# Kernel tuning notes

Hardware: AMD Instinct MI355X
Metric: run time of the kernel (lower is better)

## Reference

```python
import jax, jax.numpy as jnp
import numpy as np

B, N, F, G, H = 8, 1024, 512, 128, 8
D = F // H  # head_dim = 64


def setup_inputs() -> dict:
    key = jax.random.key(0)
    ks = jax.random.split(key, 24)
    def lin(k, fan_in, shape):
        return jax.random.normal(k, shape, jnp.float32) / np.sqrt(fan_in)
    return {
        "features": jax.random.normal(ks[0], (B, N, F), jnp.float32),
        "geometry": jax.random.normal(ks[1], (B, N, G), jnp.float32),
        "coords": jax.random.normal(ks[2], (B, N, 3), jnp.float32),
        # nnx.MultiHeadAttention params (q/k/v/out dense, with bias)
        "wq": lin(ks[3], F, (F, F)), "bq": jnp.zeros((F,), jnp.float32),
        "wk": lin(ks[4], F, (F, F)), "bk": jnp.zeros((F,), jnp.float32),
        "wv": lin(ks[5], F, (F, F)), "bv": jnp.zeros((F,), jnp.float32),
        "wo": lin(ks[6], F, (F, F)), "bo": jnp.zeros((F,), jnp.float32),
        # geometry q/k/v linears
        "gq_w": lin(ks[7], G, (G, F)), "gq_b": jnp.zeros((F,), jnp.float32),
        "gk_w": lin(ks[8], G, (G, F)), "gk_b": jnp.zeros((F,), jnp.float32),
        "gv_w": lin(ks[9], G, (G, F)), "gv_b": jnp.zeros((F,), jnp.float32),
        # distance MLP: Linear(1->H), gelu, Linear(H->H)
        "d1_w": lin(ks[10], 1, (1, H)), "d1_b": jnp.zeros((H,), jnp.float32),
        "d2_w": lin(ks[11], H, (H, H)), "d2_b": jnp.zeros((H,), jnp.float32),
        # output projection
        "op_w": lin(ks[12], F, (F, F)), "op_b": jnp.zeros((F,), jnp.float32),
    }


def _forward(features, geometry, coords,
             wq, bq, wk, bk, wv, bv, wo, bo,
             gq_w, gq_b, gk_w, gk_b, gv_w, gv_b,
             d1_w, d1_b, d2_w, d2_b, op_w, op_b):
    scale = jnp.sqrt(jnp.float32(D))
    # --- standard multi-head self-attention branch (nnx.MultiHeadAttention) ---
    q = (features @ wq + bq).reshape(B, N, H, D)
    k = (features @ wk + bk).reshape(B, N, H, D)
    v = (features @ wv + bv).reshape(B, N, H, D)
    scores = jnp.einsum("bqhd,bkhd->bhqk", q, k) / scale
    attn = jax.nn.softmax(scores, axis=-1)
    feat_att = jnp.einsum("bhqk,bkhd->bqhd", attn, v).reshape(B, N, F)
    feat_att = feat_att @ wo + bo
    # --- geometry attention branch ---
    gq = geometry @ gq_w + gq_b
    gk = geometry @ gk_w + gk_b
    gv = geometry @ gv_w + gv_b
    g_scores = jnp.einsum("bqd,bkd->bqk", gq, gk) / scale
    # pairwise distances (B,N,N,1); clamp for sqrt-at-zero safety (diagonal)
    diff = coords[:, :, None, :] - coords[:, None, :, :]
    dist = jnp.sqrt(jnp.maximum(jnp.sum(diff * diff, -1, keepdims=True), 1e-12))
    dw = jax.nn.gelu(dist @ d1_w + d1_b) @ d2_w + d2_b  # (B,N,N,H)
    # transpose to (B,H,N,N) then mean over heads == mean over last axis
    g_scores = g_scores + jnp.mean(dw, axis=-1)
    g_attn = jax.nn.softmax(g_scores, axis=-1)
    geom_att = jnp.einsum("bqk,bkd->bqd", g_attn, gv)
    return (feat_att + geom_att) @ op_w + op_b


def reference(features, geometry, coords,
              wq, bq, wk, bk, wv, bv, wo, bo,
              gq_w, gq_b, gk_w, gk_b, gv_w, gv_b,
              d1_w, d1_b, d2_w, d2_b, op_w, op_b):
    return _forward(features, geometry, coords,
                    wq, bq, wk, bk, wv, bv, wo, bo,
                    gq_w, gq_b, gk_w, gk_b, gv_w, gv_b,
                    d1_w, d1_b, d2_w, d2_b, op_w, op_b)
```

## Files before the change

### kernel.cpp

```cpp
#include <hip/hip_runtime.h>

typedef __bf16 bf16_t;
typedef __bf16 bf16x8 __attribute__((ext_vector_type(8)));
typedef __bf16 bf16x4v __attribute__((ext_vector_type(4)));
typedef float f32x4 __attribute__((ext_vector_type(4)));

#define MFMA16(a, b, c) __builtin_amdgcn_mfma_f32_16x16x32_bf16((a), (b), (c), 0, 0, 0)

static constexpr int B_ = 8, N_ = 1024, F_ = 512, H_ = 8;
static constexpr int M_ = B_ * N_;
static constexpr float LOG2E = 1.4426950408889634f;

__device__ __forceinline__ void gl_lds16(const bf16_t* gsrc, bf16_t* ldst) {
  __builtin_amdgcn_global_load_lds(
      (const __attribute__((address_space(1))) void*)gsrc,
      (__attribute__((address_space(3))) void*)ldst, 16, 0, 0);
}

__device__ __forceinline__ float gelu_tanh(float u) {
  float g = 0.7978845608028654f * fmaf(0.044715f * u * u, u, u);
  float e = __expf(2.f * g);
  float t = 1.f - 2.f / (e + 1.f);
  return 0.5f * u * (1.f + t);
}

struct PrepArgs {
  const float *features, *geometry;
  const float *wq, *wk, *wv, *wo, *op_w;
  const float *gq_w, *gk_w, *gv_w;
  const float *bq, *bk, *bv, *gq_b, *gv_b;
  const float *d1w, *d1b, *d2w, *d2b;
  bf16_t *featBF, *geomBF, *gkwBF, *WqkvT, *GqvT, *WoT, *OpT;
  float *bqkv, *gqvb, *dlut;
};

static constexpr int PR_C0 = 4096;
static constexpr int PR_C1 = PR_C0 + 1024;
static constexpr int PR_GKC = PR_C1 + 64;
static constexpr int PR_WQ = PR_GKC + 256;
static constexpr int PR_WK = PR_WQ + 256;
static constexpr int PR_WV = PR_WK + 256;
static constexpr int PR_WO = PR_WV + 256;
static constexpr int PR_OP = PR_WO + 256;
static constexpr int PR_GQ = PR_OP + 64;
static constexpr int PR_GV = PR_GQ + 64;
static constexpr int PR_B1 = PR_GV + 6;
static constexpr int PR_B2 = PR_B1 + 4;
static constexpr int PR_LUT = PR_B2 + 16;
static constexpr int PR_TOTAL = PR_LUT;

__device__ __forceinline__ void prep_cast(const float* __restrict__ in,
                                          bf16_t* __restrict__ out, int blk) {
  int i = blk * 256 + threadIdx.x;
  float4 v = ((const float4*)in)[i];
  bf16x4v o;
  o[0] = (bf16_t)v.x; o[1] = (bf16_t)v.y; o[2] = (bf16_t)v.z; o[3] = (bf16_t)v.w;
  ((bf16x4v*)out)[i] = o;
}

__device__ __forceinline__ void prep_transpose(const float* __restrict__ W,
                                               bf16_t* __restrict__ Wt,
                                               int K, int N, int ldo, int idx,
                                               float (*t)[33]) {
  const int bx = idx & 15, by = idx >> 4;
  const int kb = by * 32, cb = bx * 32;
  const int tx = threadIdx.x & 31, ty = threadIdx.x >> 5;
#pragma unroll
  for (int i = 0; i < 4; ++i)
    t[ty * 4 + i][tx] = W[(long)(kb + ty * 4 + i) * N + cb + tx];
  __syncthreads();
#pragma unroll
  for (int i = 0; i < 4; ++i)
    Wt[(long)(cb + ty * 4 + i) * ldo + kb + tx] = (bf16_t)t[tx][ty * 4 + i];
}

__global__ __launch_bounds__(256) void k_prep(PrepArgs p) {
  __shared__ float tsh[32][33];
  const int blk = blockIdx.x;
  if (blk < PR_C0) {
    prep_cast(p.features, p.featBF, blk);
  } else if (blk < PR_C1) {
    prep_cast(p.geometry, p.geomBF, blk - PR_C0);
  } else if (blk < PR_GKC) {
    prep_cast(p.gk_w, p.gkwBF, blk - PR_C1);
  } else if (blk < PR_WQ) {
    prep_transpose(p.wq, p.WqkvT, 512, 512, 512, blk - PR_GKC, tsh);
  } else if (blk < PR_WK) {
    prep_transpose(p.wk, p.WqkvT + 512 * 512, 512, 512, 512, blk - PR_WQ, tsh);
  } else if (blk < PR_WV) {
    prep_transpose(p.wv, p.WqkvT + 1024 * 512, 512, 512, 512, blk - PR_WK, tsh);
  } else if (blk < PR_WO) {
    prep_transpose(p.wo, p.WoT, 512, 512, 512, blk - PR_WV, tsh);
  } else if (blk < PR_OP) {
    prep_transpose(p.op_w, p.OpT, 512, 512, 512, blk - PR_WO, tsh);
  } else if (blk < PR_GQ) {
    prep_transpose(p.gq_w, p.GqvT, 128, 512, 128, blk - PR_OP, tsh);
  } else if (blk < PR_GV) {
    prep_transpose(p.gv_w, p.GqvT + 512 * 128, 128, 512, 128, blk - PR_GQ, tsh);
  } else if (blk < PR_B1) {
    int i = (blk - PR_GV) * 256 + threadIdx.x;
    p.bqkv[i] = i < 512 ? p.bq[i] : (i < 1024 ? p.bk[i - 512] : p.bv[i - 1024]);
  } else if (blk < PR_B2) {
    int i = (blk - PR_B1) * 256 + threadIdx.x;
    p.gqvb[i] = i < 512 ? p.gq_b[i] : p.gv_b[i - 512];
  } else {
    int i = (blk - PR_B2) * 256 + threadIdx.x;
    float d = (i + 0.5f) * (16.f / 4096.f);
    float s = 0.f;
#pragma unroll
    for (int h = 0; h < 8; ++h) s += p.d2b[h];
    s *= 0.125f;
#pragma unroll
    for (int j = 0; j < 8; ++j) {
      float w2 = 0.f;
#pragma unroll
      for (int h = 0; h < 8; ++h) w2 += p.d2w[j * 8 + h];
      s = fmaf(gelu_tanh(fmaf(d, p.d1w[j], p.d1b[j])), w2 * 0.125f, s);
    }
    p.dlut[i] = s;
  }
}

struct GemmArgs {
  const bf16_t* A; const bf16_t* Bt;
  const float* bias; const float* addSrc; const bf16_t* addSrcB;
  const float* coords; const float* lut;
  float* outF; bf16_t* outB;
  bf16_t* outT;
  int vtileFrom;
  long strideAb; long strideBb;
  int lda, ldb, K, ldout;
  float scale;
};

__device__ __forceinline__ void gemm128_core(const GemmArgs& g, int mBase, int cBase,
                                             bf16_t (*As)[64], bf16_t (*Bs)[64]) {
  const int tid = threadIdx.x;
  const int w = tid >> 6, lane = tid & 63;
  const int lr = lane & 15, lg = lane >> 4;
  const int wr = w >> 1, wc = w & 1;
  const int batch = mBase >> 10;

  const int srow = lane >> 3;
  const int scol = (lane & 7) * 8;
  const bf16_t* Ag = g.A + (long)batch * g.strideAb +
                     (long)((mBase & 1023) + w * 32 + srow) * g.lda + scol;
  const bf16_t* Bg = g.Bt + (long)batch * g.strideBb +
                     (long)(cBase + w * 32 + srow) * g.ldb + scol;
  bf16_t* Al = &As[w * 32][0];
  bf16_t* Bl = &Bs[w * 32][0];

  f32x4 zero = {0.f, 0.f, 0.f, 0.f};
  f32x4 acc[4][4];
#pragma unroll
  for (int i = 0; i < 4; ++i)
#pragma unroll
    for (int j = 0; j < 4; ++j) acc[i][j] = zero;

  for (int k0 = 0; k0 < g.K; k0 += 64) {
#pragma unroll
    for (int is = 0; is < 4; ++is) {
      gl_lds16(Ag + (long)(is * 8) * g.lda + k0, Al + is * 8 * 64);
      gl_lds16(Bg + (long)(is * 8) * g.ldb + k0, Bl + is * 8 * 64);
    }
    __syncthreads();
#pragma unroll
    for (int ks = 0; ks < 2; ++ks) {
      bf16x8 a[4], b[4];
#pragma unroll
      for (int i = 0; i < 4; ++i) {
        a[i] = *(const bf16x8*)(&As[wr * 64 + i * 16 + lr][ks * 32 + lg * 8]);
        b[i] = *(const bf16x8*)(&Bs[wc * 64 + i * 16 + lr][ks * 32 + lg * 8]);
      }
#pragma unroll
      for (int mf = 0; mf < 4; ++mf)
#pragma unroll
        for (int nf = 0; nf < 4; ++nf)
          acc[mf][nf] = MFMA16(a[mf], b[nf], acc[mf][nf]);
    }
    __syncthreads();
  }

  const int c0 = cBase + wc * 64;
  float bias4[4];
#pragma unroll
  for (int nf = 0; nf < 4; ++nf)
    bias4[nf] = g.bias ? g.bias[c0 + nf * 16 + lr] : 0.f;
  const bool vtile = (g.outT != nullptr) && (cBase >= g.vtileFrom);
#pragma unroll
  for (int mf = 0; mf < 4; ++mf) {
    const int r0 = mBase + wr * 64 + mf * 16 + lg * 4;
    const int r0b = r0 & 1023;
#pragma unroll
    for (int nf = 0; nf < 4; ++nf) {
      const int c = c0 + nf * 16 + lr;
      if (vtile) {
        bf16x4v vv;
#pragma unroll
        for (int rg = 0; rg < 4; ++rg)
          vv[rg] = (bf16_t)(acc[mf][nf][rg] * g.scale + bias4[nf]);
        *(bf16x4v*)(&g.outT[((long)batch * 512 + (c - g.vtileFrom)) * 1024 + r0b]) = vv;
      } else {
#pragma unroll
        for (int rg = 0; rg < 4; ++rg) {
          const int r = r0 + rg;
          float v = acc[mf][nf][rg] * g.scale + bias4[nf];
          if (g.addSrc) v += g.addSrc[(long)r * g.ldout + c];
          const long oi = (long)r * g.ldout + c;
          if (g.outF) g.outF[oi] = v;
          if (g.outB) g.outB[oi] = (bf16_t)v;
        }
      }
    }
  }
}

__global__ __launch_bounds__(256) void k_gemm128_dual(GemmArgs g1, GemmArgs g2) {
  __shared__ alignas(16) bf16_t As[128][64];
  __shared__ alignas(16) bf16_t Bs[128][64];
  const int bx = blockIdx.x;
  if (bx < 768) {
    gemm128_core(g1, (bx / 12) * 128, (bx % 12) * 128, As, Bs);
  } else {
    const int i = bx - 768;
    gemm128_core(g2, (i / 8) * 128, (i % 8) * 128, As, Bs);
  }
}

__device__ __forceinline__ void gemm128_dist(const GemmArgs& g, int mBase, int cBase,
                                             char* smemc) {
  bf16_t (*As)[64] = (bf16_t (*)[64])smemc;
  bf16_t (*Bs)[64] = (bf16_t (*)[64])(smemc + 16384);
  bf16_t* Lut = (bf16_t*)(smemc + 32768);
  const int tid = threadIdx.x;
  const int w = tid >> 6, lane = tid & 63;
  const int lr = lane & 15, lg = lane >> 4;
  const int wr = w >> 1, wc = w & 1;
  const int batch = mBase >> 10;

  {
    const float4* src = (const float4*)g.lut;
#pragma unroll
    for (int i = 0; i < 4; ++i) {
      float4 v = src[tid + i * 256];
      bf16x4v o;
      o[0] = (bf16_t)(v.x * LOG2E); o[1] = (bf16_t)(v.y * LOG2E);
      o[2] = (bf16_t)(v.z * LOG2E); o[3] = (bf16_t)(v.w * LOG2E);
      ((bf16x4v*)Lut)[tid + i * 256] = o;
    }
  }

  const int srow = lane >> 3;
  const int scol = (lane & 7) * 8;
  const bf16_t* Ag = g.A + (long)batch * g.strideAb +
                     (long)((mBase & 1023) + w * 32 + srow) * g.lda + scol;
  const bf16_t* Bg = g.Bt + (long)batch * g.strideBb +
                     (long)(cBase + w * 32 + srow) * g.ldb + scol;
  bf16_t* Al = &As[w * 32][0];
  bf16_t* Bl = &Bs[w * 32][0];

  f32x4 zero = {0.f, 0.f, 0.f, 0.f};
  f32x4 acc[4][4];
#pragma unroll
  for (int i = 0; i < 4; ++i)
#pragma unroll
    for (int j = 0; j < 4; ++j) acc[i][j] = zero;

  for (int k0 = 0; k0 < g.K; k0 += 64) {
#pragma unroll
    for (int is = 0; is < 4; ++is) {
      gl_lds16(Ag + (long)(is * 8) * g.lda + k0, Al + is * 8 * 64);
      gl_lds16(Bg + (long)(is * 8) * g.ldb + k0, Bl + is * 8 * 64);
    }
    __syncthreads();
#pragma unroll
    for (int ks = 0; ks < 2; ++ks) {
      bf16x8 a[4], b[4];
#pragma unroll
      for (int i = 0; i < 4; ++i) {
        a[i] = *(const bf16x8*)(&As[wr * 64 + i * 16 + lr][ks * 32 + lg * 8]);
        b[i] = *(const bf16x8*)(&Bs[wc * 64 + i * 16 + lr][ks * 32 + lg * 8]);
      }
#pragma unroll
      for (int mf = 0; mf < 4; ++mf)
#pragma unroll
        for (int nf = 0; nf < 4; ++nf)
          acc[mf][nf] = MFMA16(a[mf], b[nf], acc[mf][nf]);
    }
    __syncthreads();
  }

  const int c0 = cBase + wc * 64;
  float ckx[4], cky[4], ckz[4];
#pragma unroll
  for (int nf = 0; nf < 4; ++nf) {
    const float* ck = g.coords + ((long)batch * 1024 + c0 + nf * 16 + lr) * 3;
    ckx[nf] = ck[0]; cky[nf] = ck[1]; ckz[nf] = ck[2];
  }
#pragma unroll
  for (int mf = 0; mf < 4; ++mf) {
    const int r0 = mBase + wr * 64 + mf * 16 + lg * 4;
    float cqx[4], cqy[4], cqz[4];
#pragma unroll
    for (int rg = 0; rg < 4; ++rg) {
      const float* cq = g.coords + ((long)batch * 1024 + ((r0 + rg) & 1023)) * 3;
      cqx[rg] = cq[0]; cqy[rg] = cq[1]; cqz[rg] = cq[2];
    }
#pragma unroll
    for (int nf = 0; nf < 4; ++nf) {
      const int c = c0 + nf * 16 + lr;
#pragma unroll
      for (int rg = 0; rg < 4; ++rg) {
        const int r = r0 + rg;
        float v = acc[mf][nf][rg] * g.scale;
        float dx = cqx[rg] - ckx[nf], dy = cqy[rg] - cky[nf], dz = cqz[rg] - ckz[nf];
        float d = sqrtf(fmaxf(dx * dx + dy * dy + dz * dz, 1e-12f));
        int idx = (int)(d * 256.f);
        idx = idx > 4095 ? 4095 : idx;
        g.outB[(long)r * g.ldout + c] = (bf16_t)exp2f(v + (float)Lut[idx]);
      }
    }
  }
}

__device__ __forceinline__ void flash_core(const bf16_t* __restrict__ QKV,
                                           const bf16_t* __restrict__ Vt,
                                           bf16_t* __restrict__ fatt,
                                           int qx, int bh, char* smemc) {
  bf16_t (*Ks)[64][64] = (bf16_t (*)[64][64])smemc;
  bf16_t (*Vs)[64][64] = (bf16_t (*)[64][64])(smemc + 16384);
  char* Plb = smemc + 32768;
  const int wave = threadIdx.x >> 6, lane = threadIdx.x & 63;
  const int lr = lane & 15, lg = (lane >> 4) & 3;
  const int b = bh >> 3, h = bh & 7;
  const int qbase = qx * 64 + wave * 16;

  const bf16_t* Qb = QKV + (long)b * 1024 * 1536 + h * 64;
  const bf16_t* Kb = Qb + 512;
  const bf16_t* Vg = Vt + ((long)b * 512 + h * 64) * 1024;

  constexpr float SCL = 0.18033688011112042f;
  bf16x8 q_[2];
#pragma unroll
  for (int dh = 0; dh < 2; ++dh) {
    bf16x8 raw = *(const bf16x8*)(Qb + (long)(qbase + lr) * 1536 + dh * 32 + lg * 8);
#pragma unroll
    for (int j = 0; j < 8; ++j) q_[dh][j] = (bf16_t)((float)raw[j] * SCL);
  }
  bf16x8 onesb;
#pragma unroll
  for (int j = 0; j < 8; ++j) onesb[j] = (bf16_t)1.0f;

  const int srow = lane >> 3;
  const int scol = (((lane & 7) ^ srow) << 3);
  const bf16_t* KgB = Kb + (long)(wave * 16 + srow) * 1536 + scol;
  const bf16_t* VgB = Vg + (long)(wave * 16 + srow) * 1024 + scol;

  auto stage = [&](int buf, int kt) {
#pragma unroll
    for (int i = 0; i < 2; ++i) {
      gl_lds16(KgB + (long)(kt + i * 8) * 1536, &Ks[buf][wave * 16 + i * 8][0]);
      gl_lds16(VgB + (long)(i * 8) * 1024 + kt, &Vs[buf][wave * 16 + i * 8][0]);
    }
  };

  f32x4 zero = {0.f, 0.f, 0.f, 0.f};
  f32x4 oacc[4] = {zero, zero, zero, zero};
  f32x4 oL = zero;
  const int swz = (lr & 7) << 4;
  char* PlW = Plb + wave * 1280;

  stage(0, 0);
  asm volatile("s_waitcnt vmcnt(0)" ::: "memory");
  __syncthreads();

  auto tile = [&](const int buf, int t) __attribute__((always_inline)) {
    if (t < 15) stage(buf ^ 1, (t + 1) * 64);
    const char* KB = (const char*)&Ks[buf][0][0];
    const char* VB = (const char*)&Vs[buf][0][0];
#pragma unroll
    for (int kk = 0; kk < 2; ++kk) {
      f32x4 S[2];
      __builtin_amdgcn_s_setprio(1);
#pragma unroll
      for (int kh = 0; kh < 2; ++kh) {
        const int row = kk * 32 + kh * 16 + lr;
        bf16x8 k0 = *(const bf16x8*)(KB + row * 128 + ((lg * 16) ^ swz));
        bf16x8 k1 = *(const bf16x8*)(KB + row * 128 + ((64 + lg * 16) ^ swz));
        f32x4 tt = MFMA16(k0, q_[0], zero);
        S[kh] = MFMA16(k1, q_[1], tt);
      }
      __builtin_amdgcn_s_setprio(0);
#pragma unroll
      for (int kh = 0; kh < 2; ++kh) {
        bf16x4v pp;
#pragma unroll
        for (int r = 0; r < 4; ++r) pp[r] = (bf16_t)exp2f(S[kh][r]);
        *(bf16x4v*)(PlW + lr * 80 + kh * 32 + lg * 8) = pp;
      }
      asm volatile("s_waitcnt lgkmcnt(0)" ::: "memory");
      const bf16x8 pa = *(const bf16x8*)(PlW + lr * 80 + lg * 16);
      __builtin_amdgcn_s_setprio(1);
#pragma unroll
      for (int ct = 0; ct < 4; ++ct) {
        const int vrow = ct * 16 + lr;
        bf16x8 vf = *(const bf16x8*)(VB + vrow * 128 + ((kk * 64 + lg * 16) ^ swz));
        oacc[ct] = MFMA16(pa, vf, oacc[ct]);
      }
      oL = MFMA16(pa, onesb, oL);
      __builtin_amdgcn_s_setprio(0);
    }
    asm volatile("s_waitcnt vmcnt(0)" ::: "memory");
    __syncthreads();
  };

  for (int tt = 0; tt < 8; ++tt) {
    tile(0, tt * 2);
    tile(1, tt * 2 + 1);
  }

#pragma unroll
  for (int r = 0; r < 4; ++r) {
    float inv = 1.f / oL[r];
    int q = qbase + lg * 4 + r;
    bf16_t* orow = fatt + ((long)b * 1024 + q) * 512 + h * 64;
#pragma unroll
    for (int ct = 0; ct < 4; ++ct)
      orow[ct * 16 + lr] = (bf16_t)(oacc[ct][r] * inv);
  }
}

__global__ __launch_bounds__(256) void k_gsc_flash(GemmArgs g,
                                                   const bf16_t* __restrict__ QKV,
                                                   const bf16_t* __restrict__ Vt,
                                                   bf16_t* __restrict__ fatt) {
  __shared__ alignas(16) char smem[40960];
  const int bx = blockIdx.x;
  if (bx < 512) {
    gemm128_dist(g, (bx >> 3) * 128, (bx & 7) * 128, smem);
  } else {
    const int fid = bx - 512;
    flash_core(QKV, Vt, fatt, fid & 15, fid >> 4, smem);
  }
}

template <int RSUM>
__device__ __forceinline__ void m64_loop(const GemmArgs& g, int mBase, int cBase,
                                         bf16_t (*As)[64], bf16_t (*Bs)[64],
                                         f32x4 (*acc)[2], f32x4* lacc) {
  const int tid = threadIdx.x;
  const int w = tid >> 6, lane = tid & 63;
  const int lr = lane & 15, lg = lane >> 4;
  const int wr = w >> 1, wc = w & 1;
  const int batch = mBase >> 10;

  const int srow = lane >> 3;
  const int scol = (lane & 7) * 8;
  const bf16_t* Ag = g.A + (long)batch * g.strideAb +
                     (long)((mBase & 1023) + w * 16 + srow) * g.lda + scol;
  const bf16_t* Bg = g.Bt + (long)batch * g.strideBb +
                     (long)(cBase + w * 16 + srow) * g.ldb + scol;
  bf16_t* Al = &As[w * 16][0];
  bf16_t* Bl = &Bs[w * 16][0];

  bf16x8 onesb;
#pragma unroll
  for (int j = 0; j < 8; ++j) onesb[j] = (bf16_t)1.0f;

  for (int k0 = 0; k0 < g.K; k0 += 64) {
#pragma unroll
    for (int is = 0; is < 2; ++is) {
      gl_lds16(Ag + (long)(is * 8) * g.lda + k0, Al + is * 8 * 64);
      gl_lds16(Bg + (long)(is * 8) * g.ldb + k0, Bl + is * 8 * 64);
    }
    __syncthreads();
#pragma unroll
    for (int ks = 0; ks < 2; ++ks) {
      bf16x8 a[2], b[2];
#pragma unroll
      for (int i = 0; i < 2; ++i) {
        a[i] = *(const bf16x8*)(&As[wr * 32 + i * 16 + lr][ks * 32 + lg * 8]);
        b[i] = *(const bf16x8*)(&Bs[wc * 32 + i * 16 + lr][ks * 32 + lg * 8]);
      }
#pragma unroll
      for (int mf = 0; mf < 2; ++mf)
#pragma unroll
        for (int nf = 0; nf < 2; ++nf)
          acc[mf][nf] = MFMA16(a[mf], b[nf], acc[mf][nf]);
      if constexpr (RSUM) {
#pragma unroll
        for (int mf = 0; mf < 2; ++mf)
          lacc[mf] = MFMA16(a[mf], onesb, lacc[mf]);
      }
    }
    __syncthreads();
  }
}

__global__ __launch_bounds__(256) void k_gemm_m64(GemmArgs g) {
  __shared__ alignas(16) bf16_t As[64][64];
  __shared__ alignas(16) bf16_t Bs[64][64];
  const int tid = threadIdx.x;
  const int w = tid >> 6, lane = tid & 63;
  const int lr = lane & 15, lg = lane >> 4;
  const int wr = w >> 1, wc = w & 1;
  const int mBase = blockIdx.y * 64, cBase = blockIdx.x * 64;

  f32x4 zero = {0.f, 0.f, 0.f, 0.f};
  f32x4 acc[2][2] = {{zero, zero}, {zero, zero}};
  m64_loop<0>(g, mBase, cBase, As, Bs, acc, nullptr);

  const int c0 = cBase + wc * 32;
  float bias2[2];
#pragma unroll
  for (int nf = 0; nf < 2; ++nf)
    bias2[nf] = g.bias ? g.bias[c0 + nf * 16 + lr] : 0.f;
#pragma unroll
  for (int mf = 0; mf < 2; ++mf) {
    const int r0 = mBase + wr * 32 + mf * 16 + lg * 4;
#pragma unroll
    for (int nf = 0; nf < 2; ++nf) {
      const int c = c0 + nf * 16 + lr;
#pragma unroll
      for (int rg = 0; rg < 4; ++rg) {
        const int r = r0 + rg;
        float v = acc[mf][nf][rg] * g.scale + bias2[nf];
        const long oi = (long)r * g.ldout + c;
        if (g.outF) g.outF[oi] = v;
        if (g.outB) g.outB[oi] = (bf16_t)v;
      }
    }
  }
}

__global__ __launch_bounds__(256) void k_comb(GemmArgs gF, GemmArgs gG,
                                              bf16_t* __restrict__ outB) {
  __shared__ alignas(16) bf16_t As[64][64];
  __shared__ alignas(16) bf16_t Bs[64][64];
  const int tid = threadIdx.x;
  const int w = tid >> 6, lane = tid & 63;
  const int lr = lane & 15, lg = lane >> 4;
  const int wr = w >> 1, wc = w & 1;
  const int mBase = blockIdx.y * 64, cBase = blockIdx.x * 64;

  f32x4 zero = {0.f, 0.f, 0.f, 0.f};
  f32x4 acc1[2][2] = {{zero, zero}, {zero, zero}};
  f32x4 acc2[2][2] = {{zero, zero}, {zero, zero}};
  f32x4 lacc[2] = {zero, zero};
  m64_loop<0>(gF, mBase, cBase, As, Bs, acc1, nullptr);
  m64_loop<1>(gG, mBase, cBase, As, Bs, acc2, lacc);

  const int c0 = cBase + wc * 32;
  float bias2[2];
#pragma unroll
  for (int nf = 0; nf < 2; ++nf)
    bias2[nf] = gF.bias[c0 + nf * 16 + lr];
#pragma unroll
  for (int mf = 0; mf < 2; ++mf) {
    const int r0 = mBase + wr * 32 + mf * 16 + lg * 4;
    float linv[4];
#pragma unroll
    for (int rg = 0; rg < 4; ++rg) linv[rg] = 1.f / lacc[mf][rg];
#pragma unroll
    for (int nf = 0; nf < 2; ++nf) {
      const int c = c0 + nf * 16 + lr;
#pragma unroll
      for (int rg = 0; rg < 4; ++rg) {
        const int r = r0 + rg;
        float v = acc2[mf][nf][rg] * linv[rg] + acc1[mf][nf][rg] + bias2[nf];
        outB[(long)r * 512 + c] = (bf16_t)v;
      }
    }
  }
}

extern "C" void kernel_launch(void* const* d_in, const int* in_sizes, int n_in,
                              void* d_out, int out_size, void* d_ws, size_t ws_size,
                              hipStream_t stream) {
  const float* features = (const float*)d_in[0];
  const float* geometry = (const float*)d_in[1];
  const float* coords   = (const float*)d_in[2];
  const float* wq = (const float*)d_in[3];  const float* bq = (const float*)d_in[4];
  const float* wk = (const float*)d_in[5];  const float* bk = (const float*)d_in[6];
  const float* wv = (const float*)d_in[7];  const float* bv = (const float*)d_in[8];
  const float* wo = (const float*)d_in[9];  const float* bo = (const float*)d_in[10];
  const float* gq_w = (const float*)d_in[11]; const float* gq_b = (const float*)d_in[12];
  const float* gk_w = (const float*)d_in[13]; const float* gk_b = (const float*)d_in[14];
  const float* gv_w = (const float*)d_in[15]; const float* gv_b = (const float*)d_in[16];
  const float* d1_w = (const float*)d_in[17]; const float* d1_b = (const float*)d_in[18];
  const float* d2_w = (const float*)d_in[19]; const float* d2_b = (const float*)d_in[20];
  const float* op_w = (const float*)d_in[21]; const float* op_b = (const float*)d_in[22];
  (void)gk_b;

  size_t off = 0;
  auto carve = [&](size_t bytes) {
    void* p = (char*)d_ws + off;
    off += (bytes + 255) & ~(size_t)255;
    return p;
  };
  bf16_t* featBF = (bf16_t*)carve((size_t)M_ * F_ * 2);
  bf16_t* geomBF = (bf16_t*)carve((size_t)M_ * 128 * 2);
  bf16_t* gkwBF  = (bf16_t*)carve((size_t)128 * 512 * 2);
  bf16_t* WqkvT  = (bf16_t*)carve((size_t)1536 * 512 * 2);
  bf16_t* GqvT   = (bf16_t*)carve((size_t)1024 * 128 * 2);
  bf16_t* WoT    = (bf16_t*)carve((size_t)512 * 512 * 2);
  bf16_t* OpT    = (bf16_t*)carve((size_t)512 * 512 * 2);
  float*  bqkv   = (float*)carve(1536 * 4);
  float*  gqvb   = (float*)carve(1024 * 4);
  float*  dlut   = (float*)carve(4096 * 4);
  bf16_t* QKV    = (bf16_t*)carve((size_t)M_ * 1536 * 2);
  bf16_t* GQV    = (bf16_t*)carve((size_t)M_ * 1024 * 2);
  bf16_t* GQeff  = (bf16_t*)carve((size_t)M_ * 128 * 2);
  bf16_t* Vt     = (bf16_t*)carve((size_t)B_ * 512 * 1024 * 2);
  bf16_t* GVt    = (bf16_t*)carve((size_t)B_ * 512 * 1024 * 2);
  bf16_t* Pun    = (bf16_t*)carve((size_t)M_ * 1024 * 2);
  bf16_t* fatt   = (bf16_t*)carve((size_t)M_ * 512 * 2);
  bf16_t* combB  = (bf16_t*)carve((size_t)M_ * 512 * 2);
  if (off > ws_size) return;

  PrepArgs p;
  p.features = features; p.geometry = geometry;
  p.wq = wq; p.wk = wk; p.wv = wv; p.wo = wo; p.op_w = op_w;
  p.gq_w = gq_w; p.gk_w = gk_w; p.gv_w = gv_w;
  p.bq = bq; p.bk = bk; p.bv = bv; p.gq_b = gq_b; p.gv_b = gv_b;
  p.d1w = d1_w; p.d1b = d1_b; p.d2w = d2_w; p.d2b = d2_b;
  p.featBF = featBF; p.geomBF = geomBF; p.gkwBF = gkwBF; p.WqkvT = WqkvT;
  p.GqvT = GqvT; p.WoT = WoT; p.OpT = OpT;
  p.bqkv = bqkv; p.gqvb = gqvb; p.dlut = dlut;
  k_prep<<<PR_TOTAL, 256, 0, stream>>>(p);

  auto mk = [](const bf16_t* A, long sAb, int lda, const bf16_t* Bt, long sBb, int ldb,
               int K, const float* bias, const float* addSrc, const bf16_t* addSrcB,
               float* outF, bf16_t* outB, int ldout, float scale,
               const float* coords, const float* lut, bf16_t* outT, int vtileFrom) {
    GemmArgs g;
    g.A = A; g.Bt = Bt; g.bias = bias; g.addSrc = addSrc; g.addSrcB = addSrcB;
    g.coords = coords; g.lut = lut; g.outF = outF; g.outB = outB; g.outT = outT;
    g.vtileFrom = vtileFrom;
    g.strideAb = sAb; g.strideBb = sBb; g.lda = lda; g.ldb = ldb;
    g.K = K; g.ldout = ldout; g.scale = scale;
    return g;
  };

  k_gemm128_dual<<<1280, 256, 0, stream>>>(
      mk(featBF, (long)1024 * 512, 512, WqkvT, 0, 512, 512,
         bqkv, nullptr, nullptr, nullptr, QKV, 1536, 1.f, nullptr, nullptr, Vt, 1024),
      mk(geomBF, (long)1024 * 128, 128, GqvT, 0, 128, 128,
         gqvb, nullptr, nullptr, nullptr, GQV, 1024, 1.f, nullptr, nullptr, GVt, 512));
  k_gemm_m64<<<dim3(2, 128), 256, 0, stream>>>(
      mk(GQV, (long)1024 * 1024, 1024, gkwBF, 0, 512, 512,
         nullptr, nullptr, nullptr, nullptr, GQeff, 128, 1.f, nullptr, nullptr,
         nullptr, 1 << 30));
  k_gsc_flash<<<1536, 256, 0, stream>>>(
      mk(GQeff, (long)1024 * 128, 128, geomBF, (long)1024 * 128, 128, 128,
         nullptr, nullptr, nullptr, nullptr, Pun, 1024, 0.125f * LOG2E,
         coords, dlut, nullptr, 1 << 30),
      QKV, Vt, fatt);
  k_comb<<<dim3(8, 128), 256, 0, stream>>>(
      mk(fatt, (long)1024 * 512, 512, WoT, 0, 512, 512,
         bo, nullptr, nullptr, nullptr, nullptr, 512, 1.f, nullptr, nullptr,
         nullptr, 1 << 30),
      mk(Pun, (long)1024 * 1024, 1024, GVt, (long)512 * 1024, 1024, 1024,
         nullptr, nullptr, nullptr, nullptr, nullptr, 512, 1.f, nullptr, nullptr,
         nullptr, 1 << 30),
      combB);
  k_gemm_m64<<<dim3(8, 128), 256, 0, stream>>>(
      mk(combB, (long)1024 * 512, 512, OpT, 0, 512, 512,
         op_b, nullptr, nullptr, (float*)d_out, nullptr, 512, 1.f, nullptr, nullptr,
         nullptr, 1 << 30));
}
```

Baseline: 166.7 us.

## Fold gq and gk weights into a single 128x128 effective projection

Precomputes Weff = gk_w·gq_wᵀ and beff = gk_w·gq_b inside the prep kernel with a small MFMA tile GEMM. The geometry query then projects directly to a 128-wide GQeff in the dual GEMM alongside GV, instead of materialising a 512-wide GQ and running a separate GEMM back down to 128. This removes one kernel launch, the GQV intermediate buffer and most of the geometry projection FLOPs. The cost is extra prep work, and rounding the folded weights to bf16 changes numerics slightly.

```diff
diff --git a/kernel.cpp b/kernel.cpp
--- a/kernel.cpp
+++ b/kernel.cpp
@@ -30,22 +30,22 @@
   const float *gq_w, *gk_w, *gv_w;
   const float *bq, *bk, *bv, *gq_b, *gv_b;
   const float *d1w, *d1b, *d2w, *d2b;
-  bf16_t *featBF, *geomBF, *gkwBF, *WqkvT, *GqvT, *WoT, *OpT;
-  float *bqkv, *gqvb, *dlut;
+  bf16_t *featBF, *geomBF, *WqkvT, *GqvT2, *WoT, *OpT;
+  float *bqkv, *gqvb2, *dlut;
 };
 
 static constexpr int PR_C0 = 4096;
 static constexpr int PR_C1 = PR_C0 + 1024;
-static constexpr int PR_GKC = PR_C1 + 64;
-static constexpr int PR_WQ = PR_GKC + 256;
+static constexpr int PR_WQ = PR_C1 + 256;
 static constexpr int PR_WK = PR_WQ + 256;
 static constexpr int PR_WV = PR_WK + 256;
 static constexpr int PR_WO = PR_WV + 256;
 static constexpr int PR_OP = PR_WO + 256;
-static constexpr int PR_GQ = PR_OP + 64;
-static constexpr int PR_GV = PR_GQ + 64;
-static constexpr int PR_B1 = PR_GV + 6;
-static constexpr int PR_B2 = PR_B1 + 4;
+static constexpr int PR_GVT = PR_OP + 64;
+static constexpr int PR_WEFF = PR_GVT + 4;
+static constexpr int PR_BEFF = PR_WEFF + 1;
+static constexpr int PR_B1 = PR_BEFF + 6;
+static constexpr int PR_B2 = PR_B1 + 2;
 static constexpr int PR_LUT = PR_B2 + 16;
 static constexpr int PR_TOTAL = PR_LUT;
 
@@ -74,17 +74,23 @@
     Wt[(long)(cb + ty * 4 + i) * ldo + kb + tx] = (bf16_t)t[tx][ty * 4 + i];
 }
 
+__device__ __forceinline__ bf16x8 cvt2x4(float4 a, float4 b) {
+  bf16x8 v;
+  v[0] = (bf16_t)a.x; v[1] = (bf16_t)a.y; v[2] = (bf16_t)a.z; v[3] = (bf16_t)a.w;
+  v[4] = (bf16_t)b.x; v[5] = (bf16_t)b.y; v[6] = (bf16_t)b.z; v[7] = (bf16_t)b.w;
+  return v;
+}
+
 __global__ __launch_bounds__(256) void k_prep(PrepArgs p) {
-  __shared__ float tsh[32][33];
+  __shared__ alignas(16) char psh[16384];
+  float (*tsh)[33] = (float (*)[33])psh;
   const int blk = blockIdx.x;
   if (blk < PR_C0) {
     prep_cast(p.features, p.featBF, blk);
   } else if (blk < PR_C1) {
     prep_cast(p.geometry, p.geomBF, blk - PR_C0);
-  } else if (blk < PR_GKC) {
-    prep_cast(p.gk_w, p.gkwBF, blk - PR_C1);
   } else if (blk < PR_WQ) {
-    prep_transpose(p.wq, p.WqkvT, 512, 512, 512, blk - PR_GKC, tsh);
+    prep_transpose(p.wq, p.WqkvT, 512, 512, 512, blk - PR_C1, tsh);
   } else if (blk < PR_WK) {
     prep_transpose(p.wk, p.WqkvT + 512 * 512, 512, 512, 512, blk - PR_WQ, tsh);
   } else if (blk < PR_WV) {
@@ -93,16 +99,73 @@
     prep_transpose(p.wo, p.WoT, 512, 512, 512, blk - PR_WV, tsh);
   } else if (blk < PR_OP) {
     prep_transpose(p.op_w, p.OpT, 512, 512, 512, blk - PR_WO, tsh);
-  } else if (blk < PR_GQ) {
-    prep_transpose(p.gq_w, p.GqvT, 128, 512, 128, blk - PR_OP, tsh);
-  } else if (blk < PR_GV) {
-    prep_transpose(p.gv_w, p.GqvT + 512 * 128, 128, 512, 128, blk - PR_GQ, tsh);
+  } else if (blk < PR_GVT) {
+    prep_transpose(p.gv_w, p.GqvT2 + 128 * 128, 128, 512, 128, blk - PR_OP, tsh);
+  } else if (blk < PR_WEFF) {
+    bf16_t (*As)[64] = (bf16_t (*)[64])psh;
+    bf16_t (*Bs)[64] = (bf16_t (*)[64])(psh + 8192);
+    const int wb = blk - PR_GVT;
+    const int gBrow = (wb >> 1) * 64;
+    const int hBcol = (wb & 1) * 64;
+    const int tid = threadIdx.x;
+    const int w4 = tid >> 6, lane = tid & 63;
+    const int lr = lane & 15, lg = lane >> 4;
+    const int wr = w4 >> 1, wc = w4 & 1;
+    const int srow = tid >> 2, scol = (tid & 3) << 4;
+    f32x4 zero = {0.f, 0.f, 0.f, 0.f};
+    f32x4 acc[2][2] = {{zero, zero}, {zero, zero}};
+    for (int f0 = 0; f0 < 512; f0 += 64) {
+#pragma unroll
+      for (int hh = 0; hh < 2; ++hh) {
+        const long offA = (long)(gBrow + srow) * 512 + f0 + scol + hh * 8;
+        float4 a0 = *(const float4*)(p.gk_w + offA);
+        float4 a1 = *(const float4*)(p.gk_w + offA + 4);
+        *(bf16x8*)(&As[srow][scol + hh * 8]) = cvt2x4(a0, a1);
+        const long offB = (long)(hBcol + srow) * 512 + f0 + scol + hh * 8;
+        float4 b0 = *(const float4*)(p.gq_w + offB);
+        float4 b1 = *(const float4*)(p.gq_w + offB + 4);
+        *(bf16x8*)(&Bs[srow][scol + hh * 8]) = cvt2x4(b0, b1);
+      }
+      __syncthreads();
+#pragma unroll
+      for (int ks = 0; ks < 2; ++ks) {
+        bf16x8 a[2], b[2];
+#pragma unroll
+        for (int i = 0; i < 2; ++i) {
+          a[i] = *(const bf16x8*)(&As[wr * 32 + i * 16 + lr][ks * 32 + lg * 8]);
+          b[i] = *(const bf16x8*)(&Bs[wc * 32 + i * 16 + lr][ks * 32 + lg * 8]);
+        }
+#pragma unroll
+        for (int mf = 0; mf < 2; ++mf)
+#pragma unroll
+          for (int nf = 0; nf < 2; ++nf)
+            acc[mf][nf] = MFMA16(a[mf], b[nf], acc[mf][nf]);
+      }
+      __syncthreads();
+    }
+#pragma unroll
+    for (int mf = 0; mf < 2; ++mf)
+#pragma unroll
+      for (int nf = 0; nf < 2; ++nf)
+#pragma unroll
+        for (int rg = 0; rg < 4; ++rg) {
+          const int row = gBrow + wr * 32 + mf * 16 + lg * 4 + rg;
+          const int col = hBcol + wc * 32 + nf * 16 + lr;
+          p.GqvT2[(long)row * 128 + col] = (bf16_t)acc[mf][nf][rg];
+        }
+  } else if (blk < PR_BEFF) {
+    const int g = threadIdx.x;
+    if (g < 128) {
+      float s = 0.f;
+      for (int f = 0; f < 512; ++f) s = fmaf(p.gq_b[f], p.gk_w[(long)g * 512 + f], s);
+      p.gqvb2[g] = s;
+    }
   } else if (blk < PR_B1) {
-    int i = (blk - PR_GV) * 256 + threadIdx.x;
+    int i = (blk - PR_BEFF) * 256 + threadIdx.x;
     p.bqkv[i] = i < 512 ? p.bq[i] : (i < 1024 ? p.bk[i - 512] : p.bv[i - 1024]);
   } else if (blk < PR_B2) {
     int i = (blk - PR_B1) * 256 + threadIdx.x;
-    p.gqvb[i] = i < 512 ? p.gq_b[i] : p.gv_b[i - 512];
+    p.gqvb2[128 + i] = p.gv_b[i];
   } else {
     int i = (blk - PR_B2) * 256 + threadIdx.x;
     float d = (i + 0.5f) * (16.f / 4096.f);
@@ -223,7 +286,7 @@
     gemm128_core(g1, (bx / 12) * 128, (bx % 12) * 128, As, Bs);
   } else {
     const int i = bx - 768;
-    gemm128_core(g2, (i / 8) * 128, (i % 8) * 128, As, Bs);
+    gemm128_core(g2, (i / 5) * 128, (i % 5) * 128, As, Bs);
   }
 }
 
@@ -600,16 +663,14 @@
   };
   bf16_t* featBF = (bf16_t*)carve((size_t)M_ * F_ * 2);
   bf16_t* geomBF = (bf16_t*)carve((size_t)M_ * 128 * 2);
-  bf16_t* gkwBF  = (bf16_t*)carve((size_t)128 * 512 * 2);
   bf16_t* WqkvT  = (bf16_t*)carve((size_t)1536 * 512 * 2);
-  bf16_t* GqvT   = (bf16_t*)carve((size_t)1024 * 128 * 2);
+  bf16_t* GqvT2  = (bf16_t*)carve((size_t)640 * 128 * 2);
   bf16_t* WoT    = (bf16_t*)carve((size_t)512 * 512 * 2);
   bf16_t* OpT    = (bf16_t*)carve((size_t)512 * 512 * 2);
   float*  bqkv   = (float*)carve(1536 * 4);
-  float*  gqvb   = (float*)carve(1024 * 4);
+  float*  gqvb2  = (float*)carve(640 * 4);
   float*  dlut   = (float*)carve(4096 * 4);
   bf16_t* QKV    = (bf16_t*)carve((size_t)M_ * 1536 * 2);
-  bf16_t* GQV    = (bf16_t*)carve((size_t)M_ * 1024 * 2);
   bf16_t* GQeff  = (bf16_t*)carve((size_t)M_ * 128 * 2);
   bf16_t* Vt     = (bf16_t*)carve((size_t)B_ * 512 * 1024 * 2);
   bf16_t* GVt    = (bf16_t*)carve((size_t)B_ * 512 * 1024 * 2);
@@ -624,9 +685,9 @@
   p.gq_w = gq_w; p.gk_w = gk_w; p.gv_w = gv_w;
   p.bq = bq; p.bk = bk; p.bv = bv; p.gq_b = gq_b; p.gv_b = gv_b;
   p.d1w = d1_w; p.d1b = d1_b; p.d2w = d2_w; p.d2b = d2_b;
-  p.featBF = featBF; p.geomBF = geomBF; p.gkwBF = gkwBF; p.WqkvT = WqkvT;
-  p.GqvT = GqvT; p.WoT = WoT; p.OpT = OpT;
-  p.bqkv = bqkv; p.gqvb = gqvb; p.dlut = dlut;
+  p.featBF = featBF; p.geomBF = geomBF; p.WqkvT = WqkvT; p.GqvT2 = GqvT2;
+  p.WoT = WoT; p.OpT = OpT;
+  p.bqkv = bqkv; p.gqvb2 = gqvb2; p.dlut = dlut;
   k_prep<<<PR_TOTAL, 256, 0, stream>>>(p);
 
   auto mk = [](const bf16_t* A, long sAb, int lda, const bf16_t* Bt, long sBb, int ldb,
@@ -642,15 +703,11 @@
     return g;
   };
 
-  k_gemm128_dual<<<1280, 256, 0, stream>>>(
+  k_gemm128_dual<<<1088, 256, 0, stream>>>(
       mk(featBF, (long)1024 * 512, 512, WqkvT, 0, 512, 512,
          bqkv, nullptr, nullptr, nullptr, QKV, 1536, 1.f, nullptr, nullptr, Vt, 1024),
-      mk(geomBF, (long)1024 * 128, 128, GqvT, 0, 128, 128,
-         gqvb, nullptr, nullptr, nullptr, GQV, 1024, 1.f, nullptr, nullptr, GVt, 512));
-  k_gemm_m64<<<dim3(2, 128), 256, 0, stream>>>(
-      mk(GQV, (long)1024 * 1024, 1024, gkwBF, 0, 512, 512,
-         nullptr, nullptr, nullptr, nullptr, GQeff, 128, 1.f, nullptr, nullptr,
-         nullptr, 1 << 30));
+      mk(geomBF, (long)1024 * 128, 128, GqvT2, 0, 128, 128,
+         gqvb2, nullptr, nullptr, nullptr, GQeff, 128, 1.f, nullptr, nullptr, GVt, 128));
   k_gsc_flash<<<1536, 256, 0, stream>>>(
       mk(GQeff, (long)1024 * 128, 128, geomBF, (long)1024 * 128, 128, 128,
          nullptr, nullptr, nullptr, nullptr, Pun, 1024, 0.125f * LOG2E,
```

After: 168.1 us. About the same (+0.9%).
